# Kernel optimization log

Measured on AMD Instinct MI355X. Metric: run time of the kernel, lower is better.

Reference implementation:

```python
import jax, jax.numpy as jnp
import numpy as np

TOP_K = 4
ALPHA = 1.702
LIMIT = 7.0


def _glu(x):
    # interleaved gate/up split, clamp, custom swiglu
    gate = x[..., ::2]
    up = x[..., 1::2]
    gate = jnp.minimum(gate, LIMIT)
    up = jnp.clip(up, -LIMIT, LIMIT)
    glu = gate * jax.nn.sigmoid(gate * ALPHA)
    return (up + 1.0) * glu


def setup_inputs() -> dict:
    key = jax.random.key(0)
    ks = jax.random.split(key, 7)
    B, S, H, F, E = 1, 1024, 2880, 2880, 16
    w_scale = 0.02
    return {
        "hidden_states": jax.random.normal(ks[0], (B, S, H), dtype=jnp.float32),
        "router_w": jax.random.normal(ks[1], (E, H), dtype=jnp.float32) * w_scale,
        "router_b": jax.random.normal(ks[2], (E,), dtype=jnp.float32) * w_scale,
        "gate_up_w": jax.random.normal(ks[3], (E, H, 2 * F), dtype=jnp.float32) * w_scale,
        "gate_up_b": jax.random.normal(ks[4], (E, 2 * F), dtype=jnp.float32) * w_scale,
        "down_w": jax.random.normal(ks[5], (E, F, H), dtype=jnp.float32) * w_scale,
        "down_b": jax.random.normal(ks[6], (E, H), dtype=jnp.float32) * w_scale,
    }


def reference(hidden_states, router_w, router_b, gate_up_w, gate_up_b, down_w, down_b):
    B, S, H = hidden_states.shape
    x = hidden_states.reshape(-1, H)  # [T, H]
    T = x.shape[0]

    # Router: linear + top-k + softmax over top-k values, scattered to full [T, E]
    logits = x @ router_w.T + router_b  # [T, E]
    top_v, top_i = jax.lax.top_k(logits, TOP_K)  # [T, K]
    top_v = jax.nn.softmax(top_v, axis=-1)  # normalized top-k affinities
    scores = jnp.zeros_like(logits).at[jnp.arange(T)[:, None], top_i].set(top_v)  # [T, E]

    # Expert GLU MLPs (dense over experts; zero affinity masks unselected experts)
    gu = jnp.einsum('th,ehf->etf', x, gate_up_w) + gate_up_b[:, None, :]  # [E, T, 2F]
    act = _glu(gu)  # [E, T, F]
    out_e = jnp.einsum('etf,efh->eth', act, down_w) + down_b[:, None, :]  # [E, T, H]

    # Combine weighted by router scores
    out = jnp.einsum('te,eth->th', scores, out_e)  # [T, H]
    return out.reshape(B, S, H)
```

## Files before the change

### kernel.cpp

```cpp
#include <hip/hip_runtime.h>
#include <hip/hip_bf16.h>
#include <math.h>

#define H_DIM 2880
#define F_DIM 2880
#define GU_DIM 5760
#define NE 16
#define NT 1024
#define TOPK 4
#define NIT (H_DIM / 32)

typedef float f32x4 __attribute__((ext_vector_type(4)));
typedef __bf16 bf16x8 __attribute__((ext_vector_type(8)));

__device__ __forceinline__ unsigned short f2bf(float f) {
    union { float f; unsigned u; } v; v.f = f;
    return (unsigned short)((v.u + 0x8000u) >> 16);
}
__device__ __forceinline__ unsigned pk2(float a, float b) {
    return (unsigned)f2bf(a) | ((unsigned)f2bf(b) << 16);
}
__device__ __forceinline__ void gload16(const void* gsrc, void* ldst) {
    __builtin_amdgcn_global_load_lds(
        (const __attribute__((address_space(1))) unsigned int*)gsrc,
        (__attribute__((address_space(3))) unsigned int*)ldst,
        16, 0, 0);
}

__global__ __launch_bounds__(256) void castx_kernel(const float* __restrict__ x,
                                                    unsigned short* __restrict__ xb)
{
    int i = (blockIdx.x * 256 + threadIdx.x) * 8;
    float4 a = *(const float4*)(x + i);
    float4 b = *(const float4*)(x + i + 4);
    uint4 o;
    o.x = pk2(a.x, a.y); o.y = pk2(a.z, a.w);
    o.z = pk2(b.x, b.y); o.w = pk2(b.z, b.w);
    *(uint4*)(xb + i) = o;
}

__global__ __launch_bounds__(64) void router_kernel(
    const float* __restrict__ x, const float* __restrict__ rw, const float* __restrict__ rb,
    int* counts, int* topk_idx, float* topk_score)
{
    int t = blockIdx.x, lane = threadIdx.x;
    const float* xr = x + (size_t)t * H_DIM;
    float acc[NE];
#pragma unroll
    for (int e = 0; e < NE; e++) acc[e] = 0.f;
    for (int h = lane; h < H_DIM; h += 64) {
        float xv = xr[h];
#pragma unroll
        for (int e = 0; e < NE; e++) acc[e] += xv * rw[e * H_DIM + h];
    }
    float lg[NE];
#pragma unroll
    for (int e = 0; e < NE; e++) {
        float v = acc[e];
#pragma unroll
        for (int off = 32; off > 0; off >>= 1) v += __shfl_down(v, off, 64);
        lg[e] = v;
    }
    if (lane == 0) {
#pragma unroll
        for (int e = 0; e < NE; e++) lg[e] += rb[e];
        int mask = 0; float tv[TOPK]; int ti[TOPK];
        for (int k = 0; k < TOPK; k++) {
            float best = -1e30f; int bi = 0;
            for (int e = 0; e < NE; e++)
                if (!((mask >> e) & 1) && lg[e] > best) { best = lg[e]; bi = e; }
            mask |= 1 << bi; tv[k] = best; ti[k] = bi;
        }
        float m = tv[0], s = 0.f, ex[TOPK];
        for (int k = 0; k < TOPK; k++) { ex[k] = expf(tv[k] - m); s += ex[k]; }
        float inv = 1.f / s;
        for (int k = 0; k < TOPK; k++) {
            topk_idx[t * TOPK + k] = ti[k];
            topk_score[t * TOPK + k] = ex[k] * inv;
            atomicAdd(&counts[ti[k]], 1);
        }
    }
}

__global__ void offsets_kernel(const int* counts, int* offsets) {
    if (threadIdx.x == 0 && blockIdx.x == 0) {
        int s = 0;
        for (int e = 0; e < NE; e++) { offsets[e] = s; s += counts[e]; }
        offsets[NE] = s;
    }
}

__global__ void scatter_kernel(const int* topk_idx, const float* topk_score,
                               const int* offsets, int* fills, int* entry, float* entry_score,
                               int* slot_map)
{
    int t = blockIdx.x * blockDim.x + threadIdx.x;
    if (t >= NT) return;
    for (int k = 0; k < TOPK; k++) {
        int e = topk_idx[t * TOPK + k];
        int pos = atomicAdd(&fills[e], 1);
        int i = offsets[e] + pos;
        entry[i] = t | (k << 16);
        entry_score[i] = topk_score[t * TOPK + k];
        slot_map[t * TOPK + k] = i;
    }
}

__global__ __launch_bounds__(512) void gemm1_kernel(
    const unsigned short* __restrict__ xb, const float* __restrict__ gw, const float* __restrict__ gb,
    const int* __restrict__ counts, const int* __restrict__ offsets,
    const int* __restrict__ entry, unsigned short* __restrict__ act)
{
    int e = blockIdx.z;
    int cnt = counts[e];
    int m0 = blockIdx.y * 256;
    if (m0 >= cnt) return;
    int n0 = blockIdx.x * 128;
    int off = offsets[e];

    __shared__ __align__(16) unsigned short As[2][256 * 32];
    __shared__ __align__(16) unsigned short Bs[2][128 * 40];
    __shared__ int toks[256];

    int tid = threadIdx.x;
    if (tid < 256) {
        int r = m0 + tid;
        toks[tid] = entry[off + (r < cnt ? r : 0)] & 0xFFFF;
    }
    __syncthreads();

    int wv = tid >> 6, lane = tid & 63;

    int ar0 = 32 * wv + (lane >> 2);
    int ar1 = ar0 + 16;
    int ac = lane & 3;
    const unsigned short* asrc0 = xb + (size_t)toks[ar0] * H_DIM + 8 * (ac ^ ((ar0 >> 1) & 3));
    const unsigned short* asrc1 = xb + (size_t)toks[ar1] * H_DIM + 8 * (ac ^ ((ar1 >> 1) & 3));
    int aoff0 = (32 * wv) * 32;
    int aoff1 = (32 * wv + 16) * 32;

    int n4 = tid & 31, kb = (tid >> 5) & 7;
    const float* bptr = gw + (size_t)e * H_DIM * GU_DIM + (size_t)kb * 4 * GU_DIM + n0 + n4 * 4;
    int bwr[4];
#pragma unroll
    for (int c = 0; c < 4; c++) {
        int nl = n4 * 4 + c;
        bwr[c] = nl * 40 + (((kb >> 1) ^ ((nl >> 2) & 3)) * 8) + (kb & 1) * 4;
    }

    int wm = (wv >> 1) * 64, wn = (wv & 1) * 64;
    int r16 = lane & 15, q = lane >> 4;

    f32x4 acc[4][4] = {};
    int a_rd[4], b_rd[4];
#pragma unroll
    for (int i = 0; i < 4; i++) {
        int m = wm + i * 16 + r16;
        a_rd[i] = m * 32 + ((q ^ ((m >> 1) & 3)) * 8);
        int n = wn + i * 16 + r16;
        b_rd[i] = n * 40 + ((q ^ ((n >> 2) & 3)) * 8);
    }

    gload16(asrc0, &As[0][aoff0]);
    gload16(asrc1, &As[0][aoff1]);
    if (tid < 256) {
        float bvf[4][4];
#pragma unroll
        for (int j = 0; j < 4; j++) {
            float4 tv = *(const float4*)(bptr + (size_t)j * GU_DIM);
            bvf[j][0] = tv.x; bvf[j][1] = tv.y; bvf[j][2] = tv.z; bvf[j][3] = tv.w;
        }
#pragma unroll
        for (int c = 0; c < 4; c++)
            *(uint2*)&Bs[0][bwr[c]] = make_uint2(pk2(bvf[0][c], bvf[1][c]), pk2(bvf[2][c], bvf[3][c]));
    }
    __syncthreads();

    for (int it = 0; it < NIT; it++) {
        int cur = it & 1, nxt = cur ^ 1;
        int k1 = (it + 1) * 32;
        bool more = (it + 1 < NIT);
        float bvf[4][4];
        if (more) {
            gload16(asrc0 + k1, &As[nxt][aoff0]);
            gload16(asrc1 + k1, &As[nxt][aoff1]);
            if (tid < 256) {
#pragma unroll
                for (int j = 0; j < 4; j++) {
                    float4 tv = *(const float4*)(bptr + (size_t)(k1 + j) * GU_DIM);
                    bvf[j][0] = tv.x; bvf[j][1] = tv.y; bvf[j][2] = tv.z; bvf[j][3] = tv.w;
                }
            }
        }
        bf16x8 af[4], bq[4];
#pragma unroll
        for (int i = 0; i < 4; i++) af[i] = *(const bf16x8*)&As[cur][a_rd[i]];
#pragma unroll
        for (int i = 0; i < 4; i++) bq[i] = *(const bf16x8*)&Bs[cur][b_rd[i]];
#pragma unroll
        for (int mi = 0; mi < 4; mi++)
#pragma unroll
            for (int ni = 0; ni < 4; ni++)
                acc[mi][ni] = __builtin_amdgcn_mfma_f32_16x16x32_bf16(af[mi], bq[ni], acc[mi][ni], 0, 0, 0);
        if (more && tid < 256) {
#pragma unroll
            for (int c = 0; c < 4; c++)
                *(uint2*)&Bs[nxt][bwr[c]] = make_uint2(pk2(bvf[0][c], bvf[1][c]), pk2(bvf[2][c], bvf[3][c]));
        }
        __syncthreads();
    }

    const float* gbp = gb + (size_t)e * GU_DIM;
#pragma unroll
    for (int ni = 0; ni < 4; ni++) {
        int col = n0 + wn + ni * 16 + r16;
        float bias = gbp[col];
#pragma unroll
        for (int mi = 0; mi < 4; mi++) {
#pragma unroll
            for (int r = 0; r < 4; r++) {
                float v = acc[mi][ni][r] + bias;
                float vo = __shfl_xor(v, 1, 64);
                float gate = (lane & 1) ? vo : v;
                float up   = (lane & 1) ? v  : vo;
                gate = fminf(gate, 7.0f);
                up = fminf(fmaxf(up, -7.0f), 7.0f);
                float glu = gate / (1.0f + expf(-1.702f * gate));
                float a = (up + 1.0f) * glu;
                int row = m0 + wm + mi * 16 + q * 4 + r;
                if (row < cnt && !(lane & 1))
                    act[(size_t)(off + row) * F_DIM + (col >> 1)] = f2bf(a);
            }
        }
    }
}

__global__ __launch_bounds__(512) void gemm2_kernel(
    const unsigned short* __restrict__ act, const float* __restrict__ dw, const float* __restrict__ db,
    const int* __restrict__ counts, const int* __restrict__ offsets,
    const float* __restrict__ entry_score, float* __restrict__ slot_out)
{
    int e = blockIdx.z;
    int cnt = counts[e];
    int m0 = blockIdx.y * 256;
    if (m0 >= cnt) return;
    int n0 = blockIdx.x * 128;
    int off = offsets[e];

    __shared__ __align__(16) unsigned short As[2][256 * 32];
    __shared__ __align__(16) unsigned short Bs[2][128 * 40];
    __shared__ float scs[256];

    int tid = threadIdx.x;
    if (tid < 256) {
        int r = m0 + tid;
        scs[tid] = entry_score[off + (r < cnt ? r : 0)];
    }
    __syncthreads();

    int wv = tid >> 6, lane = tid & 63;

    int ar0 = 32 * wv + (lane >> 2);
    int ar1 = ar0 + 16;
    int ac = lane & 3;
    const unsigned short* asrc0 = act + (size_t)(off + m0 + ar0) * F_DIM + 8 * (ac ^ ((ar0 >> 1) & 3));
    const unsigned short* asrc1 = act + (size_t)(off + m0 + ar1) * F_DIM + 8 * (ac ^ ((ar1 >> 1) & 3));
    int aoff0 = (32 * wv) * 32;
    int aoff1 = (32 * wv + 16) * 32;

    int n4 = tid & 31, kb = (tid >> 5) & 7;
    int ncol = n0 + n4 * 4;
    bool nval = ncol < H_DIM;
    const float* bptr = dw + (size_t)e * F_DIM * H_DIM + (size_t)kb * 4 * H_DIM + ncol;
    int bwr[4];
#pragma unroll
    for (int c = 0; c < 4; c++) {
        int nl = n4 * 4 + c;
        bwr[c] = nl * 40 + (((kb >> 1) ^ ((nl >> 2) & 3)) * 8) + (kb & 1) * 4;
    }

    int wm = (wv >> 1) * 64, wn = (wv & 1) * 64;
    int r16 = lane & 15, q = lane >> 4;

    f32x4 acc[4][4] = {};
    int a_rd[4], b_rd[4];
#pragma unroll
    for (int i = 0; i < 4; i++) {
        int m = wm + i * 16 + r16;
        a_rd[i] = m * 32 + ((q ^ ((m >> 1) & 3)) * 8);
        int n = wn + i * 16 + r16;
        b_rd[i] = n * 40 + ((q ^ ((n >> 2) & 3)) * 8);
    }

    gload16(asrc0, &As[0][aoff0]);
    gload16(asrc1, &As[0][aoff1]);
    if (tid < 256) {
        float bvf[4][4];
#pragma unroll
        for (int j = 0; j < 4; j++) {
            float4 tv = nval ? *(const float4*)(bptr + (size_t)j * H_DIM)
                             : make_float4(0.f, 0.f, 0.f, 0.f);
            bvf[j][0] = tv.x; bvf[j][1] = tv.y; bvf[j][2] = tv.z; bvf[j][3] = tv.w;
        }
#pragma unroll
        for (int c = 0; c < 4; c++)
            *(uint2*)&Bs[0][bwr[c]] = make_uint2(pk2(bvf[0][c], bvf[1][c]), pk2(bvf[2][c], bvf[3][c]));
    }
    __syncthreads();

    for (int it = 0; it < NIT; it++) {
        int cur = it & 1, nxt = cur ^ 1;
        int k1 = (it + 1) * 32;
        bool more = (it + 1 < NIT);
        float bvf[4][4];
        if (more) {
            gload16(asrc0 + k1, &As[nxt][aoff0]);
            gload16(asrc1 + k1, &As[nxt][aoff1]);
            if (tid < 256) {
#pragma unroll
                for (int j = 0; j < 4; j++) {
                    float4 tv = nval ? *(const float4*)(bptr + (size_t)(k1 + j) * H_DIM)
                                     : make_float4(0.f, 0.f, 0.f, 0.f);
                    bvf[j][0] = tv.x; bvf[j][1] = tv.y; bvf[j][2] = tv.z; bvf[j][3] = tv.w;
                }
            }
        }
        bf16x8 af[4], bq[4];
#pragma unroll
        for (int i = 0; i < 4; i++) af[i] = *(const bf16x8*)&As[cur][a_rd[i]];
#pragma unroll
        for (int i = 0; i < 4; i++) bq[i] = *(const bf16x8*)&Bs[cur][b_rd[i]];
#pragma unroll
        for (int mi = 0; mi < 4; mi++)
#pragma unroll
            for (int ni = 0; ni < 4; ni++)
                acc[mi][ni] = __builtin_amdgcn_mfma_f32_16x16x32_bf16(af[mi], bq[ni], acc[mi][ni], 0, 0, 0);
        if (more && tid < 256) {
#pragma unroll
            for (int c = 0; c < 4; c++)
                *(uint2*)&Bs[nxt][bwr[c]] = make_uint2(pk2(bvf[0][c], bvf[1][c]), pk2(bvf[2][c], bvf[3][c]));
        }
        __syncthreads();
    }

    const float* dbp = db + (size_t)e * H_DIM;
#pragma unroll
    for (int ni = 0; ni < 4; ni++) {
        int col = n0 + wn + ni * 16 + r16;
        float bias = (col < H_DIM) ? dbp[col] : 0.f;
#pragma unroll
        for (int mi = 0; mi < 4; mi++) {
#pragma unroll
            for (int r = 0; r < 4; r++) {
                int lr = wm + mi * 16 + q * 4 + r;
                if (m0 + lr < cnt && col < H_DIM) {
                    float v = (acc[mi][ni][r] + bias) * scs[lr];
                    slot_out[(size_t)(off + m0 + lr) * H_DIM + col] = v;
                }
            }
        }
    }
}

__global__ __launch_bounds__(256) void gather_kernel(
    const float* __restrict__ slot_out, const int* __restrict__ slot_map,
    float* __restrict__ out)
{
    int t = blockIdx.x;
    int s0 = slot_map[t * TOPK + 0];
    int s1 = slot_map[t * TOPK + 1];
    int s2 = slot_map[t * TOPK + 2];
    int s3 = slot_map[t * TOPK + 3];
    const float* r0 = slot_out + (size_t)s0 * H_DIM;
    const float* r1 = slot_out + (size_t)s1 * H_DIM;
    const float* r2 = slot_out + (size_t)s2 * H_DIM;
    const float* r3 = slot_out + (size_t)s3 * H_DIM;
    float* op = out + (size_t)t * H_DIM;
    for (int h = threadIdx.x * 4; h < H_DIM; h += 1024) {
        f32x4 v = *(const f32x4*)(r0 + h) + *(const f32x4*)(r1 + h)
                + *(const f32x4*)(r2 + h) + *(const f32x4*)(r3 + h);
        *(f32x4*)(op + h) = v;
    }
}

extern "C" void kernel_launch(void* const* d_in, const int* in_sizes, int n_in,
                              void* d_out, int out_size, void* d_ws, size_t ws_size,
                              hipStream_t stream)
{
    const float* x  = (const float*)d_in[0];
    const float* rw = (const float*)d_in[1];
    const float* rb = (const float*)d_in[2];
    const float* gw = (const float*)d_in[3];
    const float* gb = (const float*)d_in[4];
    const float* dw = (const float*)d_in[5];
    const float* db = (const float*)d_in[6];
    float* out = (float*)d_out;

    char* ws = (char*)d_ws;
    int*   counts      = (int*)(ws);
    int*   fills       = (int*)(ws + 64);
    int*   offsets     = (int*)(ws + 128);
    int*   topk_idx    = (int*)(ws + 256);
    float* topk_score  = (float*)(ws + 16640);
    int*   entry       = (int*)(ws + 33024);
    float* entry_score = (float*)(ws + 49408);
    int*   slot_map    = (int*)(ws + 65792);
    unsigned short* act = (unsigned short*)(ws + 131072);
    unsigned short* xb  = (unsigned short*)(ws + 25198592);
    float* slot_out     = (float*)(ws + 31096832);

    hipMemsetAsync(ws, 0, 256, stream);

    castx_kernel<<<1440, 256, 0, stream>>>(x, xb);
    router_kernel<<<NT, 64, 0, stream>>>(x, rw, rb, counts, topk_idx, topk_score);
    offsets_kernel<<<1, 32, 0, stream>>>(counts, offsets);
    scatter_kernel<<<4, 256, 0, stream>>>(topk_idx, topk_score, offsets, fills, entry, entry_score, slot_map);
    gemm1_kernel<<<dim3(45, 4, NE), 512, 0, stream>>>(xb, gw, gb, counts, offsets, entry, act);
    gemm2_kernel<<<dim3(23, 4, NE), 512, 0, stream>>>(act, dw, db, counts, offsets, entry_score, slot_out);
    gather_kernel<<<NT, 256, 0, stream>>>(slot_out, slot_map, out);
}
```

Measured before the change: 2.097 ms.

## Retile expert GEMMs to 128x256 with split-K for down projection

Both grouped GEMMs change from 256x128 tiles to 128x256 tiles (M by N), so every thread now helps load the fp32 weight tile and each weight element is re-read by fewer blocks across the token dimension. The down projection splits K into two halves that write separate partial buffers, and the gather kernel sums both partials. The aim is better weight reuse, more blocks in flight and a shorter K loop, at the cost of a second partial output buffer and twice the gather reads. Launch bounds are also raised to request more resident blocks.

```diff
diff --git a/kernel.cpp b/kernel.cpp
--- a/kernel.cpp
+++ b/kernel.cpp
@@ -8,7 +8,9 @@
 #define NE 16
 #define NT 1024
 #define TOPK 4
-#define NIT (H_DIM / 32)
+#define NIT1 (H_DIM / 32)
+#define KSPLIT 1440
+#define NIT2 (KSPLIT / 32)
 
 typedef float f32x4 __attribute__((ext_vector_type(4)));
 typedef __bf16 bf16x8 __attribute__((ext_vector_type(8)));
@@ -106,24 +108,24 @@
     }
 }
 
-__global__ __launch_bounds__(512) void gemm1_kernel(
+__global__ __launch_bounds__(512, 4) void gemm1_kernel(
     const unsigned short* __restrict__ xb, const float* __restrict__ gw, const float* __restrict__ gb,
     const int* __restrict__ counts, const int* __restrict__ offsets,
     const int* __restrict__ entry, unsigned short* __restrict__ act)
 {
     int e = blockIdx.z;
     int cnt = counts[e];
-    int m0 = blockIdx.y * 256;
+    int m0 = blockIdx.y * 128;
     if (m0 >= cnt) return;
-    int n0 = blockIdx.x * 128;
+    int n0 = blockIdx.x * 256;
     int off = offsets[e];
 
-    __shared__ __align__(16) unsigned short As[2][256 * 32];
-    __shared__ __align__(16) unsigned short Bs[2][128 * 40];
-    __shared__ int toks[256];
+    __shared__ __align__(16) unsigned short As[2][128 * 32];
+    __shared__ __align__(16) unsigned short Bs[2][256 * 40];
+    __shared__ int toks[128];
 
     int tid = threadIdx.x;
-    if (tid < 256) {
+    if (tid < 128) {
         int r = m0 + tid;
         toks[tid] = entry[off + (r < cnt ? r : 0)] & 0xFFFF;
     }
@@ -131,16 +133,15 @@
 
     int wv = tid >> 6, lane = tid & 63;
 
-    int ar0 = 32 * wv + (lane >> 2);
-    int ar1 = ar0 + 16;
+    int ar = 16 * wv + (lane >> 2);
     int ac = lane & 3;
-    const unsigned short* asrc0 = xb + (size_t)toks[ar0] * H_DIM + 8 * (ac ^ ((ar0 >> 1) & 3));
-    const unsigned short* asrc1 = xb + (size_t)toks[ar1] * H_DIM + 8 * (ac ^ ((ar1 >> 1) & 3));
-    int aoff0 = (32 * wv) * 32;
-    int aoff1 = (32 * wv + 16) * 32;
-
-    int n4 = tid & 31, kb = (tid >> 5) & 7;
-    const float* bptr = gw + (size_t)e * H_DIM * GU_DIM + (size_t)kb * 4 * GU_DIM + n0 + n4 * 4;
+    const unsigned short* asrc = xb + (size_t)toks[ar] * H_DIM + 8 * (ac ^ ((ar >> 1) & 3));
+    int aoff = (16 * wv) * 32;
+
+    int n4 = tid & 63, kb = tid >> 6;
+    int ncol = n0 + n4 * 4;
+    bool nval = ncol < GU_DIM;
+    const float* bptr = gw + (size_t)e * H_DIM * GU_DIM + (size_t)kb * 4 * GU_DIM + ncol;
     int bwr[4];
 #pragma unroll
     for (int c = 0; c < 4; c++) {
@@ -148,7 +149,7 @@
         bwr[c] = nl * 40 + (((kb >> 1) ^ ((nl >> 2) & 3)) * 8) + (kb & 1) * 4;
     }
 
-    int wm = (wv >> 1) * 64, wn = (wv & 1) * 64;
+    int wm = (wv & 1) * 64, wn = (wv >> 1) * 64;
     int r16 = lane & 15, q = lane >> 4;
 
     f32x4 acc[4][4] = {};
@@ -161,13 +162,13 @@
         b_rd[i] = n * 40 + ((q ^ ((n >> 2) & 3)) * 8);
     }
 
-    gload16(asrc0, &As[0][aoff0]);
-    gload16(asrc1, &As[0][aoff1]);
-    if (tid < 256) {
+    gload16(asrc, &As[0][aoff]);
+    {
         float bvf[4][4];
 #pragma unroll
         for (int j = 0; j < 4; j++) {
-            float4 tv = *(const float4*)(bptr + (size_t)j * GU_DIM);
+            float4 tv = nval ? *(const float4*)(bptr + (size_t)j * GU_DIM)
+                             : make_float4(0.f, 0.f, 0.f, 0.f);
             bvf[j][0] = tv.x; bvf[j][1] = tv.y; bvf[j][2] = tv.z; bvf[j][3] = tv.w;
         }
 #pragma unroll
@@ -176,20 +177,18 @@
     }
     __syncthreads();
 
-    for (int it = 0; it < NIT; it++) {
+    for (int it = 0; it < NIT1; it++) {
         int cur = it & 1, nxt = cur ^ 1;
         int k1 = (it + 1) * 32;
-        bool more = (it + 1 < NIT);
+        bool more = (it + 1 < NIT1);
         float bvf[4][4];
         if (more) {
-            gload16(asrc0 + k1, &As[nxt][aoff0]);
-            gload16(asrc1 + k1, &As[nxt][aoff1]);
-            if (tid < 256) {
-#pragma unroll
-                for (int j = 0; j < 4; j++) {
-                    float4 tv = *(const float4*)(bptr + (size_t)(k1 + j) * GU_DIM);
-                    bvf[j][0] = tv.x; bvf[j][1] = tv.y; bvf[j][2] = tv.z; bvf[j][3] = tv.w;
-                }
+            gload16(asrc + k1, &As[nxt][aoff]);
+#pragma unroll
+            for (int j = 0; j < 4; j++) {
+                float4 tv = nval ? *(const float4*)(bptr + (size_t)(k1 + j) * GU_DIM)
+                                 : make_float4(0.f, 0.f, 0.f, 0.f);
+                bvf[j][0] = tv.x; bvf[j][1] = tv.y; bvf[j][2] = tv.z; bvf[j][3] = tv.w;
             }
         }
         bf16x8 af[4], bq[4];
@@ -202,7 +201,7 @@
 #pragma unroll
             for (int ni = 0; ni < 4; ni++)
                 acc[mi][ni] = __builtin_amdgcn_mfma_f32_16x16x32_bf16(af[mi], bq[ni], acc[mi][ni], 0, 0, 0);
-        if (more && tid < 256) {
+        if (more) {
 #pragma unroll
             for (int c = 0; c < 4; c++)
                 *(uint2*)&Bs[nxt][bwr[c]] = make_uint2(pk2(bvf[0][c], bvf[1][c]), pk2(bvf[2][c], bvf[3][c]));
@@ -214,7 +213,7 @@
 #pragma unroll
     for (int ni = 0; ni < 4; ni++) {
         int col = n0 + wn + ni * 16 + r16;
-        float bias = gbp[col];
+        float bias = (col < GU_DIM) ? gbp[col] : 0.f;
 #pragma unroll
         for (int mi = 0; mi < 4; mi++) {
 #pragma unroll
@@ -228,31 +227,35 @@
                 float glu = gate / (1.0f + expf(-1.702f * gate));
                 float a = (up + 1.0f) * glu;
                 int row = m0 + wm + mi * 16 + q * 4 + r;
-                if (row < cnt && !(lane & 1))
+                if (row < cnt && col < GU_DIM && !(lane & 1))
                     act[(size_t)(off + row) * F_DIM + (col >> 1)] = f2bf(a);
             }
         }
     }
 }
 
-__global__ __launch_bounds__(512) void gemm2_kernel(
+__global__ __launch_bounds__(512, 4) void gemm2_kernel(
     const unsigned short* __restrict__ act, const float* __restrict__ dw, const float* __restrict__ db,
     const int* __restrict__ counts, const int* __restrict__ offsets,
-    const float* __restrict__ entry_score, float* __restrict__ slot_out)
+    const float* __restrict__ entry_score,
+    float* __restrict__ p0, float* __restrict__ p1)
 {
     int e = blockIdx.z;
     int cnt = counts[e];
-    int m0 = blockIdx.y * 256;
+    int mt = blockIdx.y >> 1, kh = blockIdx.y & 1;
+    int m0 = mt * 128;
     if (m0 >= cnt) return;
-    int n0 = blockIdx.x * 128;
+    int n0 = blockIdx.x * 256;
+    int kbase = kh * KSPLIT;
     int off = offsets[e];
-
-    __shared__ __align__(16) unsigned short As[2][256 * 32];
-    __shared__ __align__(16) unsigned short Bs[2][128 * 40];
-    __shared__ float scs[256];
+    float* pout = kh ? p1 : p0;
+
+    __shared__ __align__(16) unsigned short As[2][128 * 32];
+    __shared__ __align__(16) unsigned short Bs[2][256 * 40];
+    __shared__ float scs[128];
 
     int tid = threadIdx.x;
-    if (tid < 256) {
+    if (tid < 128) {
         int r = m0 + tid;
         scs[tid] = entry_score[off + (r < cnt ? r : 0)];
     }
@@ -260,18 +263,15 @@
 
     int wv = tid >> 6, lane = tid & 63;
 
-    int ar0 = 32 * wv + (lane >> 2);
-    int ar1 = ar0 + 16;
+    int ar = 16 * wv + (lane >> 2);
     int ac = lane & 3;
-    const unsigned short* asrc0 = act + (size_t)(off + m0 + ar0) * F_DIM + 8 * (ac ^ ((ar0 >> 1) & 3));
-    const unsigned short* asrc1 = act + (size_t)(off + m0 + ar1) * F_DIM + 8 * (ac ^ ((ar1 >> 1) & 3));
-    int aoff0 = (32 * wv) * 32;
-    int aoff1 = (32 * wv + 16) * 32;
-
-    int n4 = tid & 31, kb = (tid >> 5) & 7;
+    const unsigned short* asrc = act + (size_t)(off + m0 + ar) * F_DIM + 8 * (ac ^ ((ar >> 1) & 3)) + kbase;
+    int aoff = (16 * wv) * 32;
+
+    int n4 = tid & 63, kb = tid >> 6;
     int ncol = n0 + n4 * 4;
     bool nval = ncol < H_DIM;
-    const float* bptr = dw + (size_t)e * F_DIM * H_DIM + (size_t)kb * 4 * H_DIM + ncol;
+    const float* bptr = dw + (size_t)e * F_DIM * H_DIM + (size_t)(kbase + kb * 4) * H_DIM + ncol;
     int bwr[4];
 #pragma unroll
     for (int c = 0; c < 4; c++) {
@@ -279,7 +279,7 @@
         bwr[c] = nl * 40 + (((kb >> 1) ^ ((nl >> 2) & 3)) * 8) + (kb & 1) * 4;
     }
 
-    int wm = (wv >> 1) * 64, wn = (wv & 1) * 64;
+    int wm = (wv & 1) * 64, wn = (wv >> 1) * 64;
     int r16 = lane & 15, q = lane >> 4;
 
     f32x4 acc[4][4] = {};
@@ -292,9 +292,8 @@
         b_rd[i] = n * 40 + ((q ^ ((n >> 2) & 3)) * 8);
     }
 
-    gload16(asrc0, &As[0][aoff0]);
-    gload16(asrc1, &As[0][aoff1]);
-    if (tid < 256) {
+    gload16(asrc, &As[0][aoff]);
+    {
         float bvf[4][4];
 #pragma unroll
         for (int j = 0; j < 4; j++) {
@@ -308,21 +307,18 @@
     }
     __syncthreads();
 
-    for (int it = 0; it < NIT; it++) {
+    for (int it = 0; it < NIT2; it++) {
         int cur = it & 1, nxt = cur ^ 1;
         int k1 = (it + 1) * 32;
-        bool more = (it + 1 < NIT);
+        bool more = (it + 1 < NIT2);
         float bvf[4][4];
         if (more) {
-            gload16(asrc0 + k1, &As[nxt][aoff0]);
-            gload16(asrc1 + k1, &As[nxt][aoff1]);
-            if (tid < 256) {
-#pragma unroll
-                for (int j = 0; j < 4; j++) {
-                    float4 tv = nval ? *(const float4*)(bptr + (size_t)(k1 + j) * H_DIM)
-                                     : make_float4(0.f, 0.f, 0.f, 0.f);
-                    bvf[j][0] = tv.x; bvf[j][1] = tv.y; bvf[j][2] = tv.z; bvf[j][3] = tv.w;
-                }
+            gload16(asrc + k1, &As[nxt][aoff]);
+#pragma unroll
+            for (int j = 0; j < 4; j++) {
+                float4 tv = nval ? *(const float4*)(bptr + (size_t)(k1 + j) * H_DIM)
+                                 : make_float4(0.f, 0.f, 0.f, 0.f);
+                bvf[j][0] = tv.x; bvf[j][1] = tv.y; bvf[j][2] = tv.z; bvf[j][3] = tv.w;
             }
         }
         bf16x8 af[4], bq[4];
@@ -335,7 +331,7 @@
 #pragma unroll
             for (int ni = 0; ni < 4; ni++)
                 acc[mi][ni] = __builtin_amdgcn_mfma_f32_16x16x32_bf16(af[mi], bq[ni], acc[mi][ni], 0, 0, 0);
-        if (more && tid < 256) {
+        if (more) {
 #pragma unroll
             for (int c = 0; c < 4; c++)
                 *(uint2*)&Bs[nxt][bwr[c]] = make_uint2(pk2(bvf[0][c], bvf[1][c]), pk2(bvf[2][c], bvf[3][c]));
@@ -347,7 +343,7 @@
 #pragma unroll
     for (int ni = 0; ni < 4; ni++) {
         int col = n0 + wn + ni * 16 + r16;
-        float bias = (col < H_DIM) ? dbp[col] : 0.f;
+        float bias = (kh == 0 && col < H_DIM) ? dbp[col] : 0.f;
 #pragma unroll
         for (int mi = 0; mi < 4; mi++) {
 #pragma unroll
@@ -355,7 +351,7 @@
                 int lr = wm + mi * 16 + q * 4 + r;
                 if (m0 + lr < cnt && col < H_DIM) {
                     float v = (acc[mi][ni][r] + bias) * scs[lr];
-                    slot_out[(size_t)(off + m0 + lr) * H_DIM + col] = v;
+                    pout[(size_t)(off + m0 + lr) * H_DIM + col] = v;
                 }
             }
         }
@@ -363,22 +359,22 @@
 }
 
 __global__ __launch_bounds__(256) void gather_kernel(
-    const float* __restrict__ slot_out, const int* __restrict__ slot_map,
-    float* __restrict__ out)
+    const float* __restrict__ p0, const float* __restrict__ p1,
+    const int* __restrict__ slot_map, float* __restrict__ out)
 {
     int t = blockIdx.x;
     int s0 = slot_map[t * TOPK + 0];
     int s1 = slot_map[t * TOPK + 1];
     int s2 = slot_map[t * TOPK + 2];
     int s3 = slot_map[t * TOPK + 3];
-    const float* r0 = slot_out + (size_t)s0 * H_DIM;
-    const float* r1 = slot_out + (size_t)s1 * H_DIM;
-    const float* r2 = slot_out + (size_t)s2 * H_DIM;
-    const float* r3 = slot_out + (size_t)s3 * H_DIM;
+    size_t r0 = (size_t)s0 * H_DIM, r1 = (size_t)s1 * H_DIM;
+    size_t r2 = (size_t)s2 * H_DIM, r3 = (size_t)s3 * H_DIM;
     float* op = out + (size_t)t * H_DIM;
     for (int h = threadIdx.x * 4; h < H_DIM; h += 1024) {
-        f32x4 v = *(const f32x4*)(r0 + h) + *(const f32x4*)(r1 + h)
-                + *(const f32x4*)(r2 + h) + *(const f32x4*)(r3 + h);
+        f32x4 v = *(const f32x4*)(p0 + r0 + h) + *(const f32x4*)(p1 + r0 + h)
+                + *(const f32x4*)(p0 + r1 + h) + *(const f32x4*)(p1 + r1 + h)
+                + *(const f32x4*)(p0 + r2 + h) + *(const f32x4*)(p1 + r2 + h)
+                + *(const f32x4*)(p0 + r3 + h) + *(const f32x4*)(p1 + r3 + h);
         *(f32x4*)(op + h) = v;
     }
 }
@@ -407,7 +403,8 @@
     int*   slot_map    = (int*)(ws + 65792);
     unsigned short* act = (unsigned short*)(ws + 131072);
     unsigned short* xb  = (unsigned short*)(ws + 25198592);
-    float* slot_out     = (float*)(ws + 31096832);
+    float* p0           = (float*)(ws + 31096832);
+    float* p1           = (float*)(ws + 78282752);
 
     hipMemsetAsync(ws, 0, 256, stream);
 
@@ -415,7 +412,7 @@
     router_kernel<<<NT, 64, 0, stream>>>(x, rw, rb, counts, topk_idx, topk_score);
     offsets_kernel<<<1, 32, 0, stream>>>(counts, offsets);
     scatter_kernel<<<4, 256, 0, stream>>>(topk_idx, topk_score, offsets, fills, entry, entry_score, slot_map);
-    gemm1_kernel<<<dim3(45, 4, NE), 512, 0, stream>>>(xb, gw, gb, counts, offsets, entry, act);
-    gemm2_kernel<<<dim3(23, 4, NE), 512, 0, stream>>>(act, dw, db, counts, offsets, entry_score, slot_out);
-    gather_kernel<<<NT, 256, 0, stream>>>(slot_out, slot_map, out);
-}
+    gemm1_kernel<<<dim3(23, 8, NE), 512, 0, stream>>>(xb, gw, gb, counts, offsets, entry, act);
+    gemm2_kernel<<<dim3(12, 16, NE), 512, 0, stream>>>(act, dw, db, counts, offsets, entry_score, p0, p1);
+    gather_kernel<<<NT, 256, 0, stream>>>(p0, p1, slot_map, out);
+}
```

Result: slower. 2.432 ms (+16.0%).
